# Kernel tuning notes

Hardware: AMD Instinct MI355X
Metric: run time of the kernel (lower is better)

The kernel has to match this reference:

```python
import jax, jax.numpy as jnp
import numpy as np
from math import sqrt

B, T, I, H, O, R = 128, 1000, 3, 512, 1, 2
NOISE_STD = 0.05
ALPHA = 0.2


def setup_inputs() -> dict:
    key = jax.random.key(0)
    ks = jax.random.split(key, 6)
    inp = jax.random.normal(ks[0], (B, T, I), dtype=jnp.float32)
    noise = jax.random.normal(ks[1], (B, T, H), dtype=jnp.float32)
    # parameters initialized as in the torch module
    wi = jax.random.normal(ks[2], (I, H), dtype=jnp.float32)
    si = jnp.ones((I,), dtype=jnp.float32)
    m = jax.random.normal(ks[3], (H, R), dtype=jnp.float32) * (1.0 / sqrt(H))
    n = jax.random.normal(ks[4], (H, R), dtype=jnp.float32) * (1.0 / sqrt(H))
    wo = jax.random.normal(ks[5], (H, O), dtype=jnp.float32) * (2.0 / H)
    so = jnp.ones((O,), dtype=jnp.float32)
    h0 = jnp.zeros((H,), dtype=jnp.float32)
    return {"input": inp, "noise": noise, "wi": wi, "si": si, "m": m,
            "n": n, "wo": wo, "so": so, "h0": h0}


def reference(input, noise, wi, si, m, n, wo, so, h0):
    # proxy parameters: wi_full = (wi.T * si).T, wo_full = wo * so
    wi_full = si[:, None] * wi          # (I, H)
    wo_full = wo * so                   # (H, O)
    batch = input.shape[0]
    h_init = jnp.broadcast_to(h0, (batch, h0.shape[0]))  # (B, H)

    def step(h, xs):
        x_t, z_t = xs                   # (B, I), (B, H)
        r = jnp.tanh(h)
        rec = (r @ n) @ m.T             # low-rank recurrence, (B, H)
        h_new = h + NOISE_STD * z_t + ALPHA * (-h + rec + x_t @ wi_full)
        out = jnp.tanh(h_new) @ wo_full  # (B, O)
        return h_new, (out, h_new)

    xs = (jnp.swapaxes(input, 0, 1), jnp.swapaxes(noise, 0, 1))  # time-major
    _, (outs, hs) = jax.lax.scan(step, h_init, xs)
    output = jnp.swapaxes(outs, 0, 1)               # (B, T, O)
    trajectories = jnp.concatenate(
        [h_init[:, None, :], jnp.swapaxes(hs, 0, 1)], axis=1)  # (B, T+1, H)
    return output, trajectories
```

## Files before the change

kernel.cpp:

```cpp
#include <hip/hip_runtime.h>
#include <stdint.h>

#define B_ 128
#define T_ 1000
#define H_ 512
#define PH 8
#define NPHASE 125

typedef float vfloat4 __attribute__((ext_vector_type(4)));
typedef float vfloat2 __attribute__((ext_vector_type(2)));

template <int CTRL>
__device__ __forceinline__ float dpp_add(float x) {
    int moved = __builtin_amdgcn_update_dpp(0, __float_as_int(x), CTRL, 0xf, 0xf, true);
    return x + __int_as_float(moved);
}

__device__ __forceinline__ void wave_reduce2(float& p0, float& p1) {
    p0 = dpp_add<0x111>(p0); p1 = dpp_add<0x111>(p1);
    p0 = dpp_add<0x112>(p0); p1 = dpp_add<0x112>(p1);
    p0 = dpp_add<0x114>(p0); p1 = dpp_add<0x114>(p1);
    p0 = dpp_add<0x118>(p0); p1 = dpp_add<0x118>(p1);
    p0 = dpp_add<0x142>(p0); p1 = dpp_add<0x142>(p1);
    p0 = dpp_add<0x143>(p0); p1 = dpp_add<0x143>(p1);
}

__device__ __forceinline__ float wave_reduce1(float p) {
    p = dpp_add<0x111>(p); p = dpp_add<0x112>(p); p = dpp_add<0x114>(p);
    p = dpp_add<0x118>(p); p = dpp_add<0x142>(p); p = dpp_add<0x143>(p);
    return p;
}

__device__ __forceinline__ float fast_tanh(float x) {
    float E = __builtin_amdgcn_exp2f(x * 2.885390081777927f);
    float r = __builtin_amdgcn_rcpf(E + 1.0f);
    return __builtin_fmaf(-2.0f, r, 1.0f);
}

#define C2_ 2.885390081777927f

__device__ __forceinline__ vfloat2 bc2(float x) { vfloat2 v = {x, x}; return v; }

__global__ __launch_bounds__(128, 1) void lowrank_rnn_kernel(
    const float* __restrict__ input,
    const float* __restrict__ noise,
    const float* __restrict__ wi,
    const float* __restrict__ si,
    const float* __restrict__ m,
    const float* __restrict__ n,
    const float* __restrict__ wo,
    const float* __restrict__ so,
    const float* __restrict__ h0,
    float* __restrict__ out)
{
    const int b    = blockIdx.x;
    const int tid  = threadIdx.x;
    const int wid  = tid >> 6;
    const int lane = tid & 63;
    const int j0   = lane * 8;

    __shared__ __align__(16) vfloat4 ub[2][PH][2][64];
    __shared__ __align__(16) vfloat4 rb[2][PH][2][64];
    __shared__ __align__(16) vfloat4 hb[2][PH][2][64];
    __shared__ __align__(16) vfloat4 rfin[2][64];
    __shared__ float os[T_ + 1];
    __shared__ int   flags[2];

    if (tid == 0) { flags[0] = 0; flags[1] = 0; }
    __syncthreads();
    volatile int* vprod = &flags[0];
    volatile int* vcons = &flags[1];

    if (wid == 1) {
        float wS0[8], wS1[8], wS2[8], wof[8];
        {
            const float so0 = so[0];
            #pragma unroll
            for (int i = 0; i < 3; ++i) {
                float s = 0.2f * si[i];
                float* dst = (i == 0) ? wS0 : (i == 1) ? wS1 : wS2;
                #pragma unroll
                for (int q = 0; q < 2; ++q) {
                    vfloat4 vw = *(const vfloat4*)(wi + i * H_ + j0 + 4 * q);
                    dst[4*q] = vw.x * s; dst[4*q+1] = vw.y * s;
                    dst[4*q+2] = vw.z * s; dst[4*q+3] = vw.w * s;
                }
            }
            #pragma unroll
            for (int q = 0; q < 2; ++q) {
                vfloat4 vw = *(const vfloat4*)(wo + j0 + 4 * q);
                wof[4*q] = vw.x * so0; wof[4*q+1] = vw.y * so0;
                wof[4*q+2] = vw.z * so0; wof[4*q+3] = vw.w * so0;
            }
        }
        const float* zb = noise + (size_t)b * T_ * H_ + j0;
        const float* xb = input + (size_t)b * T_ * 3;
        float* trajBase = out + (size_t)B_ * T_ + (size_t)b * (T_ + 1) * H_;

        {
            vfloat4 a = *(const vfloat4*)(h0 + j0);
            vfloat4 c = *(const vfloat4*)(h0 + j0 + 4);
            *(vfloat4*)(trajBase + j0)     = a;
            *(vfloat4*)(trajBase + j0 + 4) = c;
        }

        auto emit_phase = [&](int pp) {
            const int hf = pp & 1;
            #pragma unroll
            for (int s = 0; s < PH; ++s) {
                const int t = pp * PH + s;
                vfloat4 rl = rb[hf][s][0][lane];
                vfloat4 rh = rb[hf][s][1][lane];
                float p2 = rl.x * wof[0];
                p2 = __builtin_fmaf(rl.y, wof[1], p2);
                p2 = __builtin_fmaf(rl.z, wof[2], p2);
                p2 = __builtin_fmaf(rl.w, wof[3], p2);
                p2 = __builtin_fmaf(rh.x, wof[4], p2);
                p2 = __builtin_fmaf(rh.y, wof[5], p2);
                p2 = __builtin_fmaf(rh.z, wof[6], p2);
                p2 = __builtin_fmaf(rh.w, wof[7], p2);
                p2 = wave_reduce1(p2);
                if (lane == 63) os[t] = p2;
                vfloat4 hl = hb[hf][s][0][lane];
                vfloat4 hh = hb[hf][s][1][lane];
                float* tr = trajBase + (size_t)(t + 1) * H_ + j0;
                *(vfloat4*)tr       = hl;
                *(vfloat4*)(tr + 4) = hh;
            }
        };

        for (int q = 0; q < NPHASE; ++q) {
            if (q >= 2) {
                while (*vcons < q - 1) {}
                asm volatile("" ::: "memory");
            }
            vfloat4 zl[PH], zh[PH];
            #pragma unroll
            for (int s = 0; s < PH; ++s) {
                const float* g = zb + (size_t)(q * PH + s) * H_;
                zl[s] = *(const vfloat4*)g;
                zh[s] = *(const vfloat4*)(g + 4);
            }
            if (q >= 2) emit_phase(q - 2);
            const int half = q & 1;
            #pragma unroll
            for (int s = 0; s < PH; ++s) {
                const int t = q * PH + s;
                float x0 = xb[3*t], x1 = xb[3*t+1], x2 = xb[3*t+2];
                float zz[8] = {zl[s].x, zl[s].y, zl[s].z, zl[s].w,
                               zh[s].x, zh[s].y, zh[s].z, zh[s].w};
                float u[8];
                #pragma unroll
                for (int k = 0; k < 8; ++k) {
                    float xw = __builtin_fmaf(x0, wS0[k],
                               __builtin_fmaf(x1, wS1[k], x2 * wS2[k]));
                    u[k] = __builtin_fmaf(zz[k], 0.05f, xw);
                }
                vfloat4 ulo = {u[0], u[1], u[2], u[3]};
                vfloat4 uhi = {u[4], u[5], u[6], u[7]};
                ub[half][s][0][lane] = ulo;
                ub[half][s][1][lane] = uhi;
            }
            asm volatile("s_waitcnt lgkmcnt(0)" ::: "memory");
            if (lane == 0) *vprod = q + 1;
        }
        while (*vcons < NPHASE) {}
        asm volatile("" ::: "memory");
        emit_phase(NPHASE - 2);
        emit_phase(NPHASE - 1);
        while (*vcons < NPHASE + 1) {}
        asm volatile("" ::: "memory");
        {
            vfloat4 rl = rfin[0][lane], rh = rfin[1][lane];
            float p2 = rl.x * wof[0];
            p2 = __builtin_fmaf(rl.y, wof[1], p2);
            p2 = __builtin_fmaf(rl.z, wof[2], p2);
            p2 = __builtin_fmaf(rl.w, wof[3], p2);
            p2 = __builtin_fmaf(rh.x, wof[4], p2);
            p2 = __builtin_fmaf(rh.y, wof[5], p2);
            p2 = __builtin_fmaf(rh.z, wof[6], p2);
            p2 = __builtin_fmaf(rh.w, wof[7], p2);
            p2 = wave_reduce1(p2);
            if (lane == 63) os[T_] = p2;
        }
        asm volatile("s_waitcnt lgkmcnt(0)" ::: "memory");
        float* outp = out + (size_t)b * T_;
        for (int idx = lane; idx < T_; idx += 64)
            outp[idx] = os[idx + 1];
    } else {
        vfloat2 h2[4], n02[4], n12[4], m02[4], m12[4];
        {
            const float* nb = n + 2 * j0;
            const float* mb = m + 2 * j0;
            #pragma unroll
            for (int q = 0; q < 4; ++q) {
                vfloat4 vn = *(const vfloat4*)(nb + 4 * q);
                vfloat2 a = {vn.x, vn.z}; n02[q] = a;
                vfloat2 c = {vn.y, vn.w}; n12[q] = c;
                vfloat4 vm = *(const vfloat4*)(mb + 4 * q);
                vfloat2 d = {0.2f * vm.x, 0.2f * vm.z}; m02[q] = d;
                vfloat2 e = {0.2f * vm.y, 0.2f * vm.w}; m12[q] = e;
            }
            #pragma unroll
            for (int q = 0; q < 2; ++q) {
                vfloat4 vh = *(const vfloat4*)(h0 + j0 + 4 * q);
                vfloat2 lo = {vh.x, vh.y}, hi = {vh.z, vh.w};
                h2[2*q] = lo; h2[2*q+1] = hi;
            }
        }

        for (int p = 0; p < NPHASE; ++p) {
            while (*vprod < p + 1) {}
            asm volatile("" ::: "memory");
            const int half = p & 1;
            vfloat4 cul = ub[half][0][0][lane];
            vfloat4 cuh = ub[half][0][1][lane];
            #pragma unroll
            for (int s = 0; s < PH; ++s) {
                vfloat4 nul, nuh;
                if (s < PH - 1) {
                    nul = ub[half][s+1][0][lane];
                    nuh = ub[half][s+1][1][lane];
                }
                vfloat2 r2[4];
                #pragma unroll
                for (int j = 0; j < 4; ++j) {
                    vfloat2 x2 = h2[j] * C2_;
                    vfloat2 E  = {__builtin_amdgcn_exp2f(x2.x),
                                  __builtin_amdgcn_exp2f(x2.y)};
                    vfloat2 D  = E + 1.0f;
                    vfloat2 R  = {__builtin_amdgcn_rcpf(D.x),
                                  __builtin_amdgcn_rcpf(D.y)};
                    r2[j] = bc2(-2.0f) * R + 1.0f;
                }
                vfloat2 A0 = r2[1] * n02[1] + r2[0] * n02[0];
                vfloat2 B0 = r2[3] * n02[3] + r2[2] * n02[2];
                vfloat2 P0 = A0 + B0;
                float p0 = P0.x + P0.y;
                vfloat2 A1 = r2[1] * n12[1] + r2[0] * n12[0];
                vfloat2 B1 = r2[3] * n12[3] + r2[2] * n12[2];
                vfloat2 P1 = A1 + B1;
                float p1 = P1.x + P1.y;

                wave_reduce2(p0, p1);

                vfloat2 u2[4];
                vfloat2 t0 = {cul.x, cul.y}; u2[0] = t0;
                vfloat2 t1 = {cul.z, cul.w}; u2[1] = t1;
                vfloat2 t2 = {cuh.x, cuh.y}; u2[2] = t2;
                vfloat2 t3 = {cuh.z, cuh.w}; u2[3] = t3;
                vfloat2 base2[4];
                #pragma unroll
                for (int j = 0; j < 4; ++j)
                    base2[j] = h2[j] * 0.8f + u2[j];

                float a0 = __int_as_float(__builtin_amdgcn_readlane(__float_as_int(p0), 63));
                float a1 = __int_as_float(__builtin_amdgcn_readlane(__float_as_int(p1), 63));
                vfloat2 a02 = bc2(a0), a12 = bc2(a1);
                #pragma unroll
                for (int j = 0; j < 4; ++j)
                    h2[j] = a02 * m02[j] + (a12 * m12[j] + base2[j]);

                vfloat4 rlo = {r2[0].x, r2[0].y, r2[1].x, r2[1].y};
                vfloat4 rhi = {r2[2].x, r2[2].y, r2[3].x, r2[3].y};
                rb[half][s][0][lane] = rlo;
                rb[half][s][1][lane] = rhi;
                vfloat4 hlo = {h2[0].x, h2[0].y, h2[1].x, h2[1].y};
                vfloat4 hhi = {h2[2].x, h2[2].y, h2[3].x, h2[3].y};
                hb[half][s][0][lane] = hlo;
                hb[half][s][1][lane] = hhi;

                cul = nul; cuh = nuh;
            }
            asm volatile("s_waitcnt lgkmcnt(0)" ::: "memory");
            if (lane == 0) *vcons = p + 1;
        }
        while (*vprod < NPHASE) {}
        asm volatile("" ::: "memory");
        float hfin[8] = {h2[0].x, h2[0].y, h2[1].x, h2[1].y,
                         h2[2].x, h2[2].y, h2[3].x, h2[3].y};
        float r[8];
        #pragma unroll
        for (int k = 0; k < 8; ++k) r[k] = fast_tanh(hfin[k]);
        vfloat4 rlo = {r[0], r[1], r[2], r[3]};
        vfloat4 rhi = {r[4], r[5], r[6], r[7]};
        rfin[0][lane] = rlo;
        rfin[1][lane] = rhi;
        asm volatile("s_waitcnt lgkmcnt(0)" ::: "memory");
        if (lane == 0) *vcons = NPHASE + 1;
    }
}

extern "C" void kernel_launch(void* const* d_in, const int* in_sizes, int n_in,
                              void* d_out, int out_size, void* d_ws, size_t ws_size,
                              hipStream_t stream) {
    const float* input = (const float*)d_in[0];
    const float* noise = (const float*)d_in[1];
    const float* wi    = (const float*)d_in[2];
    const float* si    = (const float*)d_in[3];
    const float* m     = (const float*)d_in[4];
    const float* n     = (const float*)d_in[5];
    const float* wo    = (const float*)d_in[6];
    const float* so    = (const float*)d_in[7];
    const float* h0    = (const float*)d_in[8];
    float* out = (float*)d_out;

    hipLaunchKernelGGL(lowrank_rnn_kernel, dim3(B_), dim3(128), 0, stream,
                       input, noise, wi, si, m, n, wo, so, h0, out);
}
```

Before: 300.3 us.

## Move tanh off the recurrence critical path with Taylor-corrected precomputed tanh

```diff
diff --git a/kernel.cpp b/kernel.cpp
--- a/kernel.cpp
+++ b/kernel.cpp
@@ -63,6 +63,7 @@
     __shared__ __align__(16) vfloat4 rb[2][PH][2][64];
     __shared__ __align__(16) vfloat4 hb[2][PH][2][64];
     __shared__ __align__(16) vfloat4 rfin[2][64];
+    __shared__ __align__(16) vfloat4 hfin[2][64];
     __shared__ float os[T_ + 1];
     __shared__ int   flags[2];
 
@@ -123,7 +124,7 @@
                 if (lane == 63) os[t] = p2;
                 vfloat4 hl = hb[hf][s][0][lane];
                 vfloat4 hh = hb[hf][s][1][lane];
-                float* tr = trajBase + (size_t)(t + 1) * H_ + j0;
+                float* tr = trajBase + (size_t)t * H_ + j0;
                 *(vfloat4*)tr       = hl;
                 *(vfloat4*)(tr + 4) = hh;
             }
@@ -182,13 +183,17 @@
             p2 = __builtin_fmaf(rh.w, wof[7], p2);
             p2 = wave_reduce1(p2);
             if (lane == 63) os[T_] = p2;
+            float* tr = trajBase + (size_t)T_ * H_ + j0;
+            *(vfloat4*)tr       = hfin[0][lane];
+            *(vfloat4*)(tr + 4) = hfin[1][lane];
         }
         asm volatile("s_waitcnt lgkmcnt(0)" ::: "memory");
         float* outp = out + (size_t)b * T_;
         for (int idx = lane; idx < T_; idx += 64)
             outp[idx] = os[idx + 1];
     } else {
-        vfloat2 h2[4], n02[4], n12[4], m02[4], m12[4];
+        vfloat2 n02[4], n12[4], m02[4], m12[4];
+        vfloat2 bP[2][4], Tc[2][4], Dc[2][4];
         {
             const float* nb = n + 2 * j0;
             const float* mb = m + 2 * j0;
@@ -205,9 +210,16 @@
             for (int q = 0; q < 2; ++q) {
                 vfloat4 vh = *(const vfloat4*)(h0 + j0 + 4 * q);
                 vfloat2 lo = {vh.x, vh.y}, hi = {vh.z, vh.w};
-                h2[2*q] = lo; h2[2*q+1] = hi;
-            }
-        }
+                bP[0][2*q] = lo; bP[0][2*q+1] = hi;
+            }
+            #pragma unroll
+            for (int j = 0; j < 4; ++j) {
+                vfloat2 T = {fast_tanh(bP[0][j].x), fast_tanh(bP[0][j].y)};
+                Tc[0][j] = T;
+                Dc[0][j] = 1.0f - T * T;
+            }
+        }
+        float a0s = 0.0f, a1s = 0.0f;
 
         for (int p = 0; p < NPHASE; ++p) {
             while (*vprod < p + 1) {}
@@ -217,21 +229,24 @@
             vfloat4 cuh = ub[half][0][1][lane];
             #pragma unroll
             for (int s = 0; s < PH; ++s) {
+                const int pp = s & 1;
+                const int np = pp ^ 1;
                 vfloat4 nul, nuh;
                 if (s < PH - 1) {
                     nul = ub[half][s+1][0][lane];
                     nuh = ub[half][s+1][1][lane];
                 }
-                vfloat2 r2[4];
+                vfloat2 a02 = bc2(a0s), a12 = bc2(a1s);
+
+                vfloat2 dl[4], r2[4], h2[4];
+                #pragma unroll
+                for (int j = 0; j < 4; ++j)
+                    dl[j] = a02 * m02[j] + a12 * m12[j];
                 #pragma unroll
                 for (int j = 0; j < 4; ++j) {
-                    vfloat2 x2 = h2[j] * C2_;
-                    vfloat2 E  = {__builtin_amdgcn_exp2f(x2.x),
-                                  __builtin_amdgcn_exp2f(x2.y)};
-                    vfloat2 D  = E + 1.0f;
-                    vfloat2 R  = {__builtin_amdgcn_rcpf(D.x),
-                                  __builtin_amdgcn_rcpf(D.y)};
-                    r2[j] = bc2(-2.0f) * R + 1.0f;
+                    vfloat2 t1 = Tc[pp][j] * dl[j];
+                    vfloat2 e  = dl[j] - t1 * dl[j];
+                    r2[j] = Dc[pp][j] * e + Tc[pp][j];
                 }
                 vfloat2 A0 = r2[1] * n02[1] + r2[0] * n02[0];
                 vfloat2 B0 = r2[3] * n02[3] + r2[2] * n02[2];
@@ -241,25 +256,30 @@
                 vfloat2 B1 = r2[3] * n12[3] + r2[2] * n12[2];
                 vfloat2 P1 = A1 + B1;
                 float p1 = P1.x + P1.y;
-
                 wave_reduce2(p0, p1);
 
                 vfloat2 u2[4];
                 vfloat2 t0 = {cul.x, cul.y}; u2[0] = t0;
-                vfloat2 t1 = {cul.z, cul.w}; u2[1] = t1;
+                vfloat2 t1v = {cul.z, cul.w}; u2[1] = t1v;
                 vfloat2 t2 = {cuh.x, cuh.y}; u2[2] = t2;
                 vfloat2 t3 = {cuh.z, cuh.w}; u2[3] = t3;
-                vfloat2 base2[4];
-                #pragma unroll
-                for (int j = 0; j < 4; ++j)
-                    base2[j] = h2[j] * 0.8f + u2[j];
-
-                float a0 = __int_as_float(__builtin_amdgcn_readlane(__float_as_int(p0), 63));
-                float a1 = __int_as_float(__builtin_amdgcn_readlane(__float_as_int(p1), 63));
-                vfloat2 a02 = bc2(a0), a12 = bc2(a1);
-                #pragma unroll
-                for (int j = 0; j < 4; ++j)
-                    h2[j] = a02 * m02[j] + (a12 * m12[j] + base2[j]);
+                #pragma unroll
+                for (int j = 0; j < 4; ++j) {
+                    h2[j] = bP[pp][j] + dl[j];
+                    bP[np][j] = h2[j] * 0.8f + u2[j];
+                }
+                #pragma unroll
+                for (int j = 0; j < 4; ++j) {
+                    vfloat2 x2 = bP[np][j] * C2_;
+                    vfloat2 E  = {__builtin_amdgcn_exp2f(x2.x),
+                                  __builtin_amdgcn_exp2f(x2.y)};
+                    vfloat2 DD = E + 1.0f;
+                    vfloat2 R  = {__builtin_amdgcn_rcpf(DD.x),
+                                  __builtin_amdgcn_rcpf(DD.y)};
+                    vfloat2 T  = bc2(-2.0f) * R + 1.0f;
+                    Tc[np][j] = T;
+                    Dc[np][j] = 1.0f - T * T;
+                }
 
                 vfloat4 rlo = {r2[0].x, r2[0].y, r2[1].x, r2[1].y};
                 vfloat4 rhi = {r2[2].x, r2[2].y, r2[3].x, r2[3].y};
@@ -270,6 +290,9 @@
                 hb[half][s][0][lane] = hlo;
                 hb[half][s][1][lane] = hhi;
 
+                a0s = __int_as_float(__builtin_amdgcn_readlane(__float_as_int(p0), 63));
+                a1s = __int_as_float(__builtin_amdgcn_readlane(__float_as_int(p1), 63));
+
                 cul = nul; cuh = nuh;
             }
             asm volatile("s_waitcnt lgkmcnt(0)" ::: "memory");
@@ -277,15 +300,24 @@
         }
         while (*vprod < NPHASE) {}
         asm volatile("" ::: "memory");
-        float hfin[8] = {h2[0].x, h2[0].y, h2[1].x, h2[1].y,
-                         h2[2].x, h2[2].y, h2[3].x, h2[3].y};
-        float r[8];
+        vfloat2 a02 = bc2(a0s), a12 = bc2(a1s);
+        float r[8], hT8[8];
         #pragma unroll
-        for (int k = 0; k < 8; ++k) r[k] = fast_tanh(hfin[k]);
+        for (int j = 0; j < 4; ++j) {
+            vfloat2 dlt = a02 * m02[j] + a12 * m12[j];
+            vfloat2 hT  = bP[0][j] + dlt;
+            hT8[2*j] = hT.x; hT8[2*j+1] = hT.y;
+            r[2*j]   = fast_tanh(hT.x);
+            r[2*j+1] = fast_tanh(hT.y);
+        }
         vfloat4 rlo = {r[0], r[1], r[2], r[3]};
         vfloat4 rhi = {r[4], r[5], r[6], r[7]};
         rfin[0][lane] = rlo;
         rfin[1][lane] = rhi;
+        vfloat4 hlo = {hT8[0], hT8[1], hT8[2], hT8[3]};
+        vfloat4 hhi = {hT8[4], hT8[5], hT8[6], hT8[7]};
+        hfin[0][lane] = hlo;
+        hfin[1][lane] = hhi;
         asm volatile("s_waitcnt lgkmcnt(0)" ::: "memory");
         if (lane == 0) *vcons = NPHASE + 1;
     }
```

New measurement: 294.5 us. About the same (-1.9%).
